# Kernel optimization log

Measured on AMD Instinct MI355X. Metric: run time of the kernel, lower is better.

The kernel has to match this reference:

```python
import jax, jax.numpy as jnp
import numpy as np

NR = 5000            # number of sampled center points
H, W = 480, 640      # depth map resolution
P = NR * (NR - 1) // 2  # number of ordered pairs (i < j) = 12,497,500


def setup_inputs() -> dict:
    key = jax.random.key(0)
    k1, k2, k3, k4 = jax.random.split(key, 4)
    x = jax.random.normal(k1, (H, W), dtype=jnp.float32)
    rows = jax.random.randint(k2, (NR,), 0, H)
    cols = jax.random.randint(k3, (NR,), 0, W)
    centers = jnp.stack([rows, cols], axis=1).astype(jnp.int32)  # [NR, 2]
    # relative-depth ground truth labels in {-1, 0, +1}; mask = |gt|
    gt = jax.random.randint(k4, (P,), -1, 2).astype(jnp.float32)
    return {"x": x, "gt": gt, "centers": centers}


def reference(x, gt, centers):
    # gather predicted depths at the NR sampled pixel locations
    z = x[centers[:, 0], centers[:, 1]]            # [NR]
    # all pairs i<j in the same row-major order as the original double loop
    ii, jj = jnp.triu_indices(NR, k=1)             # each [P]
    d = z[ii] - z[jj]                              # z_A - z_B, [P]
    mask = jnp.abs(gt)                             # [P]
    # logistic ranking loss where gt != 0, squared loss where gt == 0
    loss = mask * jnp.log1p(jnp.exp(-gt * d)) + (1.0 - mask) * d * d
    return jnp.sum(loss) / jnp.float32(P)
```

## Files before the change

kernel.cpp:

```cpp
#include <hip/hip_runtime.h>
#include <stdint.h>

#define NR 5000
#define NRM1 4999
#define W 640
#define NBLK 2500
#define NELEM 20
#define PCOUNT 12497500.0f
#define LOG2E 1.44269504088896340736f
#define LN2   0.69314718055994530942f

__global__ void gather_z(const float* __restrict__ x,
                         const int* __restrict__ centers,
                         float* __restrict__ z) {
    int t = blockIdx.x * blockDim.x + threadIdx.x;
    if (t < NR) {
        const int2 rc = ((const int2*)centers)[t];
        z[t] = x[rc.x * W + rc.y];
    }
}

__global__ __launch_bounds__(256) void pair_loss(const float* __restrict__ gt,
                                                 const float* __restrict__ z,
                                                 float* __restrict__ partials) {
    __shared__ float sz[NR];
    __shared__ float wsum[4];
    const int tid = threadIdx.x;
    const int b = blockIdx.x;

    const float4* __restrict__ zf4 = (const float4*)z;
    for (int t = tid; t < NR / 4; t += 256)
        *(float4*)&sz[4 * t] = zf4[t];
    __syncthreads();

    const int r1 = b;
    const int r2 = NR - 2 - b;
    const int len1 = NRM1 - r1;
    const int off1 = r1 * NRM1 - (r1 * (r1 - 1)) / 2;
    const int off2 = r2 * NRM1 - (r2 * (r2 - 1)) / 2;
    const int off2v = off2 - len1;
    const int vmax = (r2 > r1) ? 5000 : len1;
    const float zr1 = sz[r1];
    const float zr2 = sz[r2];

    float g[NELEM];
    int vc[NELEM];
    #pragma unroll
    for (int k = 0; k < NELEM; ++k) {
        const int v = tid + 256 * k;
        const int c = min(v, vmax - 1);
        vc[k] = c;
        const int ofs = (c < len1) ? off1 : off2v;
        g[k] = gt[ofs + c];
    }

    float a0 = 0.0f, a1 = 0.0f, a2 = 0.0f, a3 = 0.0f;
    #pragma unroll
    for (int k = 0; k < NELEM; ++k) {
        const int c = vc[k];
        const bool row1 = c < len1;
        const float zj = sz[c + (row1 ? r1 + 1 : 0)];
        const float zr = row1 ? zr1 : zr2;
        const float gg = g[k];
        const float d  = zr - zj;
        const float dl = d * LOG2E;
        const float lg = __log2f(1.0f + exp2f(-gg * dl));
        float l = (gg != 0.0f) ? lg : d * dl;
        l = (tid + 256 * k < vmax) ? l : 0.0f;
        if      ((k & 3) == 0) a0 += l;
        else if ((k & 3) == 1) a1 += l;
        else if ((k & 3) == 2) a2 += l;
        else                   a3 += l;
    }
    float acc = (a0 + a1) + (a2 + a3);

    for (int o = 32; o > 0; o >>= 1) acc += __shfl_down(acc, o, 64);
    if ((tid & 63) == 0) wsum[tid >> 6] = acc;
    __syncthreads();
    if (tid == 0)
        partials[b] = (wsum[0] + wsum[1]) + (wsum[2] + wsum[3]);
}

__global__ __launch_bounds__(256) void final_reduce(const float* __restrict__ partials,
                                                    float* __restrict__ out) {
    __shared__ float wsum[4];
    float acc = 0.0f;
    const float4* __restrict__ p4 = (const float4*)partials;
    for (int t = threadIdx.x; t < NBLK / 4; t += 256) {
        const float4 v = p4[t];
        acc += (v.x + v.y) + (v.z + v.w);
    }
    for (int o = 32; o > 0; o >>= 1) acc += __shfl_down(acc, o, 64);
    if ((threadIdx.x & 63) == 0) wsum[threadIdx.x >> 6] = acc;
    __syncthreads();
    if (threadIdx.x == 0)
        out[0] = ((wsum[0] + wsum[1]) + (wsum[2] + wsum[3])) * (LN2 / PCOUNT);
}

extern "C" void kernel_launch(void* const* d_in, const int* in_sizes, int n_in,
                              void* d_out, int out_size, void* d_ws, size_t ws_size,
                              hipStream_t stream) {
    const float* x       = (const float*)d_in[0];
    const float* gt      = (const float*)d_in[1];
    const int*   centers = (const int*)d_in[2];
    float* out = (float*)d_out;

    float* z        = (float*)d_ws;
    float* partials = z + NR;

    gather_z<<<(NR + 255) / 256, 256, 0, stream>>>(x, centers, z);
    pair_loss<<<NBLK, 256, 0, stream>>>(gt, z, partials);
    final_reduce<<<1, 256, 0, stream>>>(partials, out);
}
```

Baseline: 24.62 us.

## Drop LDS staging of z, read z from global/L2, use 128-thread blocks

Removes the per-block copy of all 5000 z values into shared memory and its barrier, reading z directly from global memory (cached) instead. Blocks shrink to 128 threads with 40 elements per thread, processed in two batches of 20 gt loads each. This avoids every block re-staging 20KB into LDS, at the cost of scattered global/L1 gathers for z and less memory-level parallelism per thread.

```diff
diff --git a/kernel.cpp b/kernel.cpp
--- a/kernel.cpp
+++ b/kernel.cpp
@@ -5,7 +5,9 @@
 #define NRM1 4999
 #define W 640
 #define NBLK 2500
-#define NELEM 20
+#define NTHR 128
+#define NELEM 40
+#define BATCH 20
 #define PCOUNT 12497500.0f
 #define LOG2E 1.44269504088896340736f
 #define LN2   0.69314718055994530942f
@@ -20,18 +22,12 @@
     }
 }
 
-__global__ __launch_bounds__(256) void pair_loss(const float* __restrict__ gt,
-                                                 const float* __restrict__ z,
-                                                 float* __restrict__ partials) {
-    __shared__ float sz[NR];
-    __shared__ float wsum[4];
+__global__ __launch_bounds__(NTHR) void pair_loss(const float* __restrict__ gt,
+                                                  const float* __restrict__ z,
+                                                  float* __restrict__ partials) {
+    __shared__ float wsum[NTHR / 64];
     const int tid = threadIdx.x;
     const int b = blockIdx.x;
-
-    const float4* __restrict__ zf4 = (const float4*)z;
-    for (int t = tid; t < NR / 4; t += 256)
-        *(float4*)&sz[4 * t] = zf4[t];
-    __syncthreads();
 
     const int r1 = b;
     const int r2 = NR - 2 - b;
@@ -40,37 +36,39 @@
     const int off2 = r2 * NRM1 - (r2 * (r2 - 1)) / 2;
     const int off2v = off2 - len1;
     const int vmax = (r2 > r1) ? 5000 : len1;
-    const float zr1 = sz[r1];
-    const float zr2 = sz[r2];
-
-    float g[NELEM];
-    int vc[NELEM];
-    #pragma unroll
-    for (int k = 0; k < NELEM; ++k) {
-        const int v = tid + 256 * k;
-        const int c = min(v, vmax - 1);
-        vc[k] = c;
-        const int ofs = (c < len1) ? off1 : off2v;
-        g[k] = gt[ofs + c];
-    }
+    const float zr1 = z[r1];
+    const float zr2 = z[r2];
 
     float a0 = 0.0f, a1 = 0.0f, a2 = 0.0f, a3 = 0.0f;
+
     #pragma unroll
-    for (int k = 0; k < NELEM; ++k) {
-        const int c = vc[k];
-        const bool row1 = c < len1;
-        const float zj = sz[c + (row1 ? r1 + 1 : 0)];
-        const float zr = row1 ? zr1 : zr2;
-        const float gg = g[k];
-        const float d  = zr - zj;
-        const float dl = d * LOG2E;
-        const float lg = __log2f(1.0f + exp2f(-gg * dl));
-        float l = (gg != 0.0f) ? lg : d * dl;
-        l = (tid + 256 * k < vmax) ? l : 0.0f;
-        if      ((k & 3) == 0) a0 += l;
-        else if ((k & 3) == 1) a1 += l;
-        else if ((k & 3) == 2) a2 += l;
-        else                   a3 += l;
+    for (int h = 0; h < NELEM / BATCH; ++h) {
+        float g[BATCH];
+        #pragma unroll
+        for (int k = 0; k < BATCH; ++k) {
+            const int v = tid + NTHR * (h * BATCH + k);
+            const int c = min(v, vmax - 1);
+            const int ofs = (c < len1) ? off1 : off2v;
+            g[k] = gt[ofs + c];
+        }
+        #pragma unroll
+        for (int k = 0; k < BATCH; ++k) {
+            const int v = tid + NTHR * (h * BATCH + k);
+            const int c = min(v, vmax - 1);
+            const bool row1 = c < len1;
+            const float zj = z[c + (row1 ? r1 + 1 : 0)];
+            const float zr = row1 ? zr1 : zr2;
+            const float gg = g[k];
+            const float d  = zr - zj;
+            const float dl = d * LOG2E;
+            const float lg = __log2f(1.0f + exp2f(-gg * dl));
+            float l = (gg != 0.0f) ? lg : d * dl;
+            l = (v < vmax) ? l : 0.0f;
+            if      ((k & 3) == 0) a0 += l;
+            else if ((k & 3) == 1) a1 += l;
+            else if ((k & 3) == 2) a2 += l;
+            else                   a3 += l;
+        }
     }
     float acc = (a0 + a1) + (a2 + a3);
 
@@ -78,15 +76,15 @@
     if ((tid & 63) == 0) wsum[tid >> 6] = acc;
     __syncthreads();
     if (tid == 0)
-        partials[b] = (wsum[0] + wsum[1]) + (wsum[2] + wsum[3]);
+        partials[b] = wsum[0] + wsum[1];
 }
 
-__global__ __launch_bounds__(256) void final_reduce(const float* __restrict__ partials,
-                                                    float* __restrict__ out) {
-    __shared__ float wsum[4];
+__global__ __launch_bounds__(NTHR) void final_reduce(const float* __restrict__ partials,
+                                                     float* __restrict__ out) {
+    __shared__ float wsum[NTHR / 64];
     float acc = 0.0f;
     const float4* __restrict__ p4 = (const float4*)partials;
-    for (int t = threadIdx.x; t < NBLK / 4; t += 256) {
+    for (int t = threadIdx.x; t < NBLK / 4; t += NTHR) {
         const float4 v = p4[t];
         acc += (v.x + v.y) + (v.z + v.w);
     }
@@ -94,7 +92,7 @@
     if ((threadIdx.x & 63) == 0) wsum[threadIdx.x >> 6] = acc;
     __syncthreads();
     if (threadIdx.x == 0)
-        out[0] = ((wsum[0] + wsum[1]) + (wsum[2] + wsum[3])) * (LN2 / PCOUNT);
+        out[0] = (wsum[0] + wsum[1]) * (LN2 / PCOUNT);
 }
 
 extern "C" void kernel_launch(void* const* d_in, const int* in_sizes, int n_in,
@@ -109,6 +107,6 @@
     float* partials = z + NR;
 
     gather_z<<<(NR + 255) / 256, 256, 0, stream>>>(x, centers, z);
-    pair_loss<<<NBLK, 256, 0, stream>>>(gt, z, partials);
-    final_reduce<<<1, 256, 0, stream>>>(partials, out);
+    pair_loss<<<NBLK, NTHR, 0, stream>>>(gt, z, partials);
+    final_reduce<<<1, NTHR, 0, stream>>>(partials, out);
 }
```

New measurement: 25.86 us. +5.0%, slower.
